# Optimization experiments

Measured on AMD Instinct MI355X. Metric: run time of the kernel, lower is better.

## Reference

```python
import jax, jax.numpy as jnp
import numpy as np

B = 131072
# join branch layer dims: 203 -> 175 -> 150 -> 128 -> 80 -> 48
DIMS = [203, 175, 150, 128, 80, 48]

def setup_inputs() -> dict:
    key = jax.random.key(0)
    ks = jax.random.split(key, 11)
    inp = {"x": jax.random.normal(ks[0], (B, DIMS[0]), dtype=jnp.float32)}
    for i in range(5):
        fan_in, fan_out = DIMS[i], DIMS[i + 1]
        bound = 1.0 / np.sqrt(fan_in)
        inp[f"W{i+1}"] = jax.random.uniform(ks[1 + 2 * i], (fan_out, fan_in), minval=-bound, maxval=bound, dtype=jnp.float32)
        inp[f"b{i+1}"] = jax.random.uniform(ks[2 + 2 * i], (fan_out,), minval=-bound, maxval=bound, dtype=jnp.float32)
    return inp

def reference(x, W1, b1, W2, b2, W3, b3, W4, b4, W5, b5):
    # join branch of NodeEmbedding, dropout in eval mode (identity).
    h = jnp.tanh(x @ W1.T + b1)      # [B,175]
    h = jnp.tanh(h @ W2.T + b2)      # [B,150]
    h = jnp.tanh(h @ W3.T + b3)      # [B,128]
    h = jnp.tanh(h @ W4.T + b4)      # [B,80]
    return h @ W5.T + b5             # [B,48], no activation on last layer
```

## Files before the change

### kernel.cpp

```cpp
#include <hip/hip_runtime.h>


typedef short short8 __attribute__((ext_vector_type(8)));
typedef float f32x16 __attribute__((ext_vector_type(16)));
typedef unsigned int uint;
typedef unsigned short ushort;

#define PSTR 116
#define NTHREADS 768
#define MROWS 64
#define BIAS_OFF (207 * 2048)

__device__ __forceinline__ ushort f2bf(float f) {
    uint u = __float_as_uint(f);
    u += 0x7FFFu + ((u >> 16) & 1u);
    return (ushort)(u >> 16);
}
__device__ __forceinline__ float bf2f(ushort h) { return __uint_as_float(((uint)h) << 16); }
__device__ __forceinline__ float fast_tanh(float x) {
    float e = __expf(2.0f * x);
    float t = __builtin_amdgcn_rcpf(e + 1.0f);
    return fmaf(-2.0f, t, 1.0f);
}
__device__ __forceinline__ uint cvt_pk_bf16(float s0, float s1) {
    uint r;
    asm("v_cvt_pk_bf16_f32 %0, %1, %2" : "=v"(r) : "v"(s0), "v"(s1));
    return r;
}

union U4S8 { uint4 u; short8 s; };

__global__ void prep_weights(const float* __restrict__ W1, const float* __restrict__ W2,
                             const float* __restrict__ W3, const float* __restrict__ W4,
                             const float* __restrict__ W5,
                             const float* __restrict__ b1, const float* __restrict__ b2,
                             const float* __restrict__ b3, const float* __restrict__ b4,
                             const float* __restrict__ b5, char* __restrict__ ws)
{
    const int b = blockIdx.x, l = threadIdx.x;
    const int FOa[5]  = {175, 150, 128, 80, 48};
    if (b == 207) {
        float* bp = (float*)(ws + BIAS_OFF);
        const float* bs[5] = {b1, b2, b3, b4, b5};
        for (int i = l; i < 5 * 192; i += 64) {
            int L = i / 192, j = i - L * 192;
            bp[i] = (j < FOa[L]) ? bs[L][j] : 0.0f;
        }
        return;
    }
    int layer, local;
    if      (b <  78) { layer = 0; local = b; }
    else if (b < 133) { layer = 1; local = b - 78; }
    else if (b < 173) { layer = 2; local = b - 133; }
    else if (b < 197) { layer = 3; local = b - 173; }
    else              { layer = 4; local = b - 197; }
    const int NTa[5]  = {6, 5, 4, 3, 2};
    const int FINa[5] = {203, 175, 150, 128, 80};
    const float* Wp = (layer == 0) ? W1 : (layer == 1) ? W2 : (layer == 2) ? W3
                    : (layer == 3) ? W4 : W5;
    const int nt = NTa[layer], fin = FINa[layer], fout = FOa[layer];
    const int c = local / nt, t = local % nt;
    const int n  = t * 32 + (l & 31);
    const int kb = c * 16 + (l >> 5) * 8;
    uint hw[4], lw[4];
#pragma unroll
    for (int j = 0; j < 8; ++j) {
        int k = kb + j;
        float v = (n < fout && k < fin) ? Wp[(size_t)n * fin + k] : 0.0f;
        ushort hh = f2bf(v);
        ushort ll = f2bf(v - bf2f(hh));
        if (j & 1) { hw[j >> 1] |= ((uint)hh) << 16; lw[j >> 1] |= ((uint)ll) << 16; }
        else       { hw[j >> 1]  = hh;               lw[j >> 1]  = ll; }
    }
    char* dst = ws + (size_t)b * 2048 + l * 16;
    *(uint4*)dst          = make_uint4(hw[0], hw[1], hw[2], hw[3]);
    *(uint4*)(dst + 1024) = make_uint4(lw[0], lw[1], lw[2], lw[3]);
}

template<int KC, int NT, int FOUT, bool ACT, bool LAST>
__device__ __forceinline__ void run_layer(const char* __restrict__ wsL,
    const float* __restrict__ biasP, uint* aH, uint* aL, float* outg,
    int row0, int l, int rg, int t, int lx, int lh)
{
    f32x16 acc;
    if (t < NT) {
        const float4* bp = (const float4*)(biasP + t * 32 + 4 * lh);
#pragma unroll
        for (int q = 0; q < 4; ++q) {
            float4 bv = bp[q * 2];
            acc[4 * q + 0] = bv.x; acc[4 * q + 1] = bv.y;
            acc[4 * q + 2] = bv.z; acc[4 * q + 3] = bv.w;
        }

        const char* ha = (const char*)aH + (rg * 32 + lx) * (PSTR * 4) + lh * 16;
        const char* la = (const char*)aL + (rg * 32 + lx) * (PSTR * 4) + lh * 16;
        const uint4* wsb = (const uint4*)wsL + (size_t)(t * 2) * 64 + l;

        U4S8 wh[3], wl[3], ah[2], al[2];
        wh[0].u = wsb[0];                  wl[0].u = wsb[64];
        wh[1].u = wsb[(size_t)NT * 128];   wl[1].u = wsb[(size_t)NT * 128 + 64];
        ah[0].u = *(const uint4*)ha;       al[0].u = *(const uint4*)la;

#pragma unroll
        for (int c = 0; c < KC; ++c) {
            if (c + 2 < KC) {
                wh[(c + 2) % 3].u = wsb[(size_t)(c + 2) * NT * 128];
                wl[(c + 2) % 3].u = wsb[(size_t)(c + 2) * NT * 128 + 64];
            }
            if (c + 1 < KC) {
                ah[(c + 1) & 1].u = *(const uint4*)(ha + (c + 1) * 32);
                al[(c + 1) & 1].u = *(const uint4*)(la + (c + 1) * 32);
            }
            __builtin_amdgcn_sched_barrier(0);
            acc = __builtin_amdgcn_mfma_f32_32x32x16_bf16(wh[c % 3].s, ah[c & 1].s, acc, 0, 0, 0);
            acc = __builtin_amdgcn_mfma_f32_32x32x16_bf16(wh[c % 3].s, al[c & 1].s, acc, 0, 0, 0);
            acc = __builtin_amdgcn_mfma_f32_32x32x16_bf16(wl[c % 3].s, ah[c & 1].s, acc, 0, 0, 0);
        }
    }
    if (!LAST) __syncthreads();

    if (t < NT) {
        const int rowb = rg * 32 + lx;
        if (LAST) {
#pragma unroll
            for (int q = 0; q < 4; ++q) {
                const int f = t * 32 + 8 * q + 4 * lh;
                if (f + 3 < 48) {
                    float4 v = make_float4(acc[4 * q], acc[4 * q + 1],
                                           acc[4 * q + 2], acc[4 * q + 3]);
                    *(float4*)(outg + (size_t)(row0 + rowb) * 48 + f) = v;
                }
            }
        } else {
            uint* pHd = aH + rowb * PSTR;
            uint* pLd = aL + rowb * PSTR;
#pragma unroll
            for (int q = 0; q < 4; ++q) {
                float t0 = acc[4 * q], t1 = acc[4 * q + 1];
                float t2 = acc[4 * q + 2], t3 = acc[4 * q + 3];
                if (ACT) { t0 = fast_tanh(t0); t1 = fast_tanh(t1);
                           t2 = fast_tanh(t2); t3 = fast_tanh(t3); }
                uint h01 = cvt_pk_bf16(t0, t1);
                uint h23 = cvt_pk_bf16(t2, t3);
                float r0 = t0 - __uint_as_float(h01 << 16);
                float r1 = t1 - __uint_as_float(h01 & 0xFFFF0000u);
                float r2 = t2 - __uint_as_float(h23 << 16);
                float r3 = t3 - __uint_as_float(h23 & 0xFFFF0000u);
                uint l01 = cvt_pk_bf16(r0, r1);
                uint l23 = cvt_pk_bf16(r2, r3);
                const int dcol = t * 16 + 4 * q + 2 * lh;
                *(uint2*)(pHd + dcol) = make_uint2(h01, h23);
                *(uint2*)(pLd + dcol) = make_uint2(l01, l23);
            }
        }
    }
    if (!LAST) __syncthreads();
}

__global__ __launch_bounds__(NTHREADS, 4)
void mlp_mfma(const float* __restrict__ x,
              const char* __restrict__ ws, float* __restrict__ out)
{
    __shared__ __align__(16) uint aH[MROWS * PSTR];
    __shared__ __align__(16) uint aL[MROWS * PSTR];

    const int tid = threadIdx.x;
    const int l = tid & 63, w = tid >> 6;
    const int rg = w / 6, t = w - 6 * rg;
    const int lx = l & 31, lh = l >> 5;
    const int row0 = blockIdx.x * MROWS;
    const float* biasT = (const float*)(ws + BIAS_OFF);

    for (int e = tid; e < MROWS * 104; e += NTHREADS) {
        int row = e / 104, dcol = e - row * 104;
        int col = dcol * 2;
        const float* xp = x + (size_t)(row0 + row) * 203;
        float v0 = (col < 203) ? xp[col] : 0.0f;
        float v1 = (col + 1 < 203) ? xp[col + 1] : 0.0f;
        uint chi = cvt_pk_bf16(v0, v1);
        float h0 = __uint_as_float(chi << 16);
        float h1 = __uint_as_float(chi & 0xFFFF0000u);
        uint clo = cvt_pk_bf16(v0 - h0, v1 - h1);
        aH[row * PSTR + dcol] = chi;
        aL[row * PSTR + dcol] = clo;
    }
    __syncthreads();

    run_layer<13, 6, 175, true,  false>(ws,              biasT,       aH, aL, nullptr, row0, l, rg, t, lx, lh);
    run_layer<11, 5, 150, true,  false>(ws +  78 * 2048, biasT + 192, aH, aL, nullptr, row0, l, rg, t, lx, lh);
    run_layer<10, 4, 128, true,  false>(ws + 133 * 2048, biasT + 384, aH, aL, nullptr, row0, l, rg, t, lx, lh);
    run_layer< 8, 3,  80, true,  false>(ws + 173 * 2048, biasT + 576, aH, aL, nullptr, row0, l, rg, t, lx, lh);
    run_layer< 5, 2,  48, false, true >(ws + 197 * 2048, biasT + 768, aH, aL, out,     row0, l, rg, t, lx, lh);
}

extern "C" void kernel_launch(void* const* d_in, const int* in_sizes, int n_in,
                              void* d_out, int out_size, void* d_ws, size_t ws_size,
                              hipStream_t stream) {
    (void)in_sizes; (void)n_in; (void)ws_size; (void)out_size;
    const float* x  = (const float*)d_in[0];
    const float* W1 = (const float*)d_in[1];
    const float* b1 = (const float*)d_in[2];
    const float* W2 = (const float*)d_in[3];
    const float* b2 = (const float*)d_in[4];
    const float* W3 = (const float*)d_in[5];
    const float* b3 = (const float*)d_in[6];
    const float* W4 = (const float*)d_in[7];
    const float* b4 = (const float*)d_in[8];
    const float* W5 = (const float*)d_in[9];
    const float* b5 = (const float*)d_in[10];
    float* out = (float*)d_out;
    char* ws = (char*)d_ws;

    hipLaunchKernelGGL(prep_weights, dim3(208), dim3(64), 0, stream,
                       W1, W2, W3, W4, W5, b1, b2, b3, b4, b5, ws);
    hipLaunchKernelGGL(mlp_mfma, dim3(131072 / MROWS), dim3(NTHREADS), 0, stream,
                       x, ws, out);
}
```

Baseline: 280.7 us.

## Shrink blocks to 32 rows with 6 waves and drop manual software pipelining

Each block now handles 32 rows with 384 threads (one row group) instead of 64 rows with two row groups, the LDS padding stride is reduced, and launch bounds target 5 blocks per CU. The explicit triple-buffered weight and double-buffered activation prefetch with sched_barrier is removed in favour of plain per-iteration loads left to the compiler to schedule. The aim is lower register and LDS use per block, and so more resident blocks to hide latency. The risk is exposed global-load latency in the MFMA loop, twice as many blocks and barriers per row, and possible LDS bank conflicts from the new stride.

```diff
diff --git a/kernel.cpp b/kernel.cpp
--- a/kernel.cpp
+++ b/kernel.cpp
@@ -6,9 +6,9 @@
 typedef unsigned int uint;
 typedef unsigned short ushort;
 
-#define PSTR 116
-#define NTHREADS 768
-#define MROWS 64
+#define PSTR 108
+#define NTHREADS 384
+#define MROWS 32
 #define BIAS_OFF (207 * 2048)
 
 __device__ __forceinline__ ushort f2bf(float f) {
@@ -77,10 +77,10 @@
     *(uint4*)(dst + 1024) = make_uint4(lw[0], lw[1], lw[2], lw[3]);
 }
 
-template<int KC, int NT, int FOUT, bool ACT, bool LAST>
+template<int KC, int NT, bool ACT, bool LAST>
 __device__ __forceinline__ void run_layer(const char* __restrict__ wsL,
     const float* __restrict__ biasP, uint* aH, uint* aL, float* outg,
-    int row0, int l, int rg, int t, int lx, int lh)
+    int row0, int l, int t, int lx, int lh)
 {
     f32x16 acc;
     if (t < NT) {
@@ -91,36 +91,24 @@
             acc[4 * q + 0] = bv.x; acc[4 * q + 1] = bv.y;
             acc[4 * q + 2] = bv.z; acc[4 * q + 3] = bv.w;
         }
-
-        const char* ha = (const char*)aH + (rg * 32 + lx) * (PSTR * 4) + lh * 16;
-        const char* la = (const char*)aL + (rg * 32 + lx) * (PSTR * 4) + lh * 16;
+        const char* ha = (const char*)aH + lx * (PSTR * 4) + lh * 16;
+        const char* la = (const char*)aL + lx * (PSTR * 4) + lh * 16;
         const uint4* wsb = (const uint4*)wsL + (size_t)(t * 2) * 64 + l;
-
-        U4S8 wh[3], wl[3], ah[2], al[2];
-        wh[0].u = wsb[0];                  wl[0].u = wsb[64];
-        wh[1].u = wsb[(size_t)NT * 128];   wl[1].u = wsb[(size_t)NT * 128 + 64];
-        ah[0].u = *(const uint4*)ha;       al[0].u = *(const uint4*)la;
-
 #pragma unroll
         for (int c = 0; c < KC; ++c) {
-            if (c + 2 < KC) {
-                wh[(c + 2) % 3].u = wsb[(size_t)(c + 2) * NT * 128];
-                wl[(c + 2) % 3].u = wsb[(size_t)(c + 2) * NT * 128 + 64];
-            }
-            if (c + 1 < KC) {
-                ah[(c + 1) & 1].u = *(const uint4*)(ha + (c + 1) * 32);
-                al[(c + 1) & 1].u = *(const uint4*)(la + (c + 1) * 32);
-            }
-            __builtin_amdgcn_sched_barrier(0);
-            acc = __builtin_amdgcn_mfma_f32_32x32x16_bf16(wh[c % 3].s, ah[c & 1].s, acc, 0, 0, 0);
-            acc = __builtin_amdgcn_mfma_f32_32x32x16_bf16(wh[c % 3].s, al[c & 1].s, acc, 0, 0, 0);
-            acc = __builtin_amdgcn_mfma_f32_32x32x16_bf16(wl[c % 3].s, ah[c & 1].s, acc, 0, 0, 0);
+            U4S8 wh, wl, ah, al;
+            wh.u = wsb[(size_t)c * NT * 128];
+            wl.u = wsb[(size_t)c * NT * 128 + 64];
+            ah.u = *(const uint4*)(ha + c * 32);
+            al.u = *(const uint4*)(la + c * 32);
+            acc = __builtin_amdgcn_mfma_f32_32x32x16_bf16(wh.s, ah.s, acc, 0, 0, 0);
+            acc = __builtin_amdgcn_mfma_f32_32x32x16_bf16(wh.s, al.s, acc, 0, 0, 0);
+            acc = __builtin_amdgcn_mfma_f32_32x32x16_bf16(wl.s, ah.s, acc, 0, 0, 0);
         }
     }
     if (!LAST) __syncthreads();
 
     if (t < NT) {
-        const int rowb = rg * 32 + lx;
         if (LAST) {
 #pragma unroll
             for (int q = 0; q < 4; ++q) {
@@ -128,12 +116,12 @@
                 if (f + 3 < 48) {
                     float4 v = make_float4(acc[4 * q], acc[4 * q + 1],
                                            acc[4 * q + 2], acc[4 * q + 3]);
-                    *(float4*)(outg + (size_t)(row0 + rowb) * 48 + f) = v;
+                    *(float4*)(outg + (size_t)(row0 + lx) * 48 + f) = v;
                 }
             }
         } else {
-            uint* pHd = aH + rowb * PSTR;
-            uint* pLd = aL + rowb * PSTR;
+            uint* pHd = aH + lx * PSTR;
+            uint* pLd = aL + lx * PSTR;
 #pragma unroll
             for (int q = 0; q < 4; ++q) {
                 float t0 = acc[4 * q], t1 = acc[4 * q + 1];
@@ -157,7 +145,7 @@
     if (!LAST) __syncthreads();
 }
 
-__global__ __launch_bounds__(NTHREADS, 4)
+__global__ __launch_bounds__(NTHREADS, 5)
 void mlp_mfma(const float* __restrict__ x,
               const char* __restrict__ ws, float* __restrict__ out)
 {
@@ -166,7 +154,6 @@
 
     const int tid = threadIdx.x;
     const int l = tid & 63, w = tid >> 6;
-    const int rg = w / 6, t = w - 6 * rg;
     const int lx = l & 31, lh = l >> 5;
     const int row0 = blockIdx.x * MROWS;
     const float* biasT = (const float*)(ws + BIAS_OFF);
@@ -186,11 +173,11 @@
     }
     __syncthreads();
 
-    run_layer<13, 6, 175, true,  false>(ws,              biasT,       aH, aL, nullptr, row0, l, rg, t, lx, lh);
-    run_layer<11, 5, 150, true,  false>(ws +  78 * 2048, biasT + 192, aH, aL, nullptr, row0, l, rg, t, lx, lh);
-    run_layer<10, 4, 128, true,  false>(ws + 133 * 2048, biasT + 384, aH, aL, nullptr, row0, l, rg, t, lx, lh);
-    run_layer< 8, 3,  80, true,  false>(ws + 173 * 2048, biasT + 576, aH, aL, nullptr, row0, l, rg, t, lx, lh);
-    run_layer< 5, 2,  48, false, true >(ws + 197 * 2048, biasT + 768, aH, aL, out,     row0, l, rg, t, lx, lh);
+    run_layer<13, 6, true,  false>(ws,              biasT,       aH, aL, nullptr, row0, l, w, lx, lh);
+    run_layer<11, 5, true,  false>(ws +  78 * 2048, biasT + 192, aH, aL, nullptr, row0, l, w, lx, lh);
+    run_layer<10, 4, true,  false>(ws + 133 * 2048, biasT + 384, aH, aL, nullptr, row0, l, w, lx, lh);
+    run_layer< 8, 3, true,  false>(ws + 173 * 2048, biasT + 576, aH, aL, nullptr, row0, l, w, lx, lh);
+    run_layer< 5, 2, false, true >(ws + 197 * 2048, biasT + 768, aH, aL, out,     row0, l, w, lx, lh);
 }
 
 extern "C" void kernel_launch(void* const* d_in, const int* in_sizes, int n_in,
```

Measured after the change: 286.4 us. 2.0% more time.
